# Performance work log

Measured on AMD Instinct MI355X. Metric: run time of the kernel, lower is better.

Reference implementation:

```python
import jax, jax.numpy as jnp
import numpy as np

POOL = 7
STRIDE = 16.0


def setup_inputs() -> dict:
    key = jax.random.key(0)
    k1, k2, k3, k4, k5 = jax.random.split(key, 5)
    image = jax.random.normal(k1, (1, 128, 128, 512), dtype=jnp.float32)
    N = 1000
    # RoIs in input-image pixel coords: (x_center, y_center, w, h)
    w = jax.random.uniform(k2, (N,), minval=32.0, maxval=480.0)
    h = jax.random.uniform(k3, (N,), minval=32.0, maxval=480.0)
    x0 = jax.random.uniform(k4, (N,), minval=0.0, maxval=1500.0)
    y0 = jax.random.uniform(k5, (N,), minval=0.0, maxval=1500.0)
    RoI = jnp.stack([x0 + w / 2, y0 + h / 2, w, h], axis=1).astype(jnp.float32)
    return {"image": image, "RoI_inImage": RoI}


def _axis_coords(start, size, pool, limit):
    """Half-pixel bilinear sample coords for resizing a [size]-long crop
    starting at `start` to `pool` samples (matches tf.image.resize bilinear).
    Returns (i0, i1, frac) each [N, pool]."""
    grid = (jnp.arange(pool, dtype=jnp.float32) + 0.5) / pool  # [pool]
    s = grid[None, :] * size[:, None] - 0.5                    # crop-relative
    s = jnp.clip(s, 0.0, size[:, None] - 1.0)
    f0 = jnp.floor(s)
    frac = s - f0
    f1 = jnp.minimum(f0 + 1.0, size[:, None] - 1.0)
    i0 = jnp.clip(start[:, None] + f0, 0, limit - 1).astype(jnp.int32)
    i1 = jnp.clip(start[:, None] + f1, 0, limit - 1).astype(jnp.int32)
    return i0, i1, frac


def _roi_pool(image, RoI):
    H, W = image.shape[1], image.shape[2]
    feat = image[0]  # [H, W, C]
    x, y, w, h = RoI[:, 0], RoI[:, 1], RoI[:, 2], RoI[:, 3]
    # integer crop bounds on the stride-16 feature map (non-differentiable)
    r = jax.lax.stop_gradient(jnp.round((x - w / 2) / STRIDE))   # col start
    c = jax.lax.stop_gradient(jnp.round((y - h / 2) / STRIDE))   # row start
    wq = jax.lax.stop_gradient(jnp.maximum(jnp.round(w / STRIDE), 1.0))
    hq = jax.lax.stop_gradient(jnp.maximum(jnp.round(h / STRIDE), 1.0))
    iy0, iy1, ly = _axis_coords(c, hq, POOL, H)  # rows   [N, P]
    ix0, ix1, lx = _axis_coords(r, wq, POOL, W)  # cols   [N, P]
    # gather 4 corners: [N, P, P, C]
    g = lambda iy, ix: feat[iy[:, :, None], ix[:, None, :]]
    ly_ = ly[:, :, None, None]
    lx_ = lx[:, None, :, None]
    out = ((1 - ly_) * (1 - lx_) * g(iy0, ix0)
           + (1 - ly_) * lx_ * g(iy0, ix1)
           + ly_ * (1 - lx_) * g(iy1, ix0)
           + ly_ * lx_ * g(iy1, ix1))
    N = RoI.shape[0]
    return out.reshape(1, N, POOL, POOL, feat.shape[-1])


def reference(image, RoI_inImage):
    return _roi_pool(image, RoI_inImage)
```

## Files before the change

### kernel.cpp

```cpp
#include <hip/hip_runtime.h>

#define POOL    7
#define RSTRIDE 16.0f
#define IMG_H   128
#define IMG_W   128
#define IMG_C   512
#define C4      (IMG_C / 4)

typedef float f4v __attribute__((ext_vector_type(4)));

template <bool SWIZZLE>
__global__ __launch_bounds__(128)
void roi_pool_kernel(const float* __restrict__ image,
                     const float* __restrict__ roi,
                     float* __restrict__ out, int N)
{
    int n, py;
    if (SWIZZLE) {
        const int per   = N >> 3;
        const int xcd   = blockIdx.x & 7;
        const int local = blockIdx.x >> 3;
        const int q     = local / POOL;
        n  = xcd * per + q;
        py = local - q * POOL;
    } else {
        n  = blockIdx.x / POOL;
        py = blockIdx.x - n * POOL;
    }

    const float x = roi[n * 4 + 0];
    const float y = roi[n * 4 + 1];
    const float w = roi[n * 4 + 2];
    const float h = roi[n * 4 + 3];

    const float r  = rintf((x - 0.5f * w) / RSTRIDE);
    const float c  = rintf((y - 0.5f * h) / RSTRIDE);
    const float wq = fmaxf(rintf(w / RSTRIDE), 1.0f);
    const float hq = fmaxf(rintf(h / RSTRIDE), 1.0f);

    float sy = (((float)py + 0.5f) / (float)POOL) * hq - 0.5f;
    sy = fminf(fmaxf(sy, 0.0f), hq - 1.0f);
    const float fy0 = floorf(sy);
    const float ly  = sy - fy0;
    const float fy1 = fminf(fy0 + 1.0f, hq - 1.0f);
    const int iy0 = (int)fminf(fmaxf(c + fy0, 0.0f), (float)(IMG_H - 1));
    const int iy1 = (int)fminf(fmaxf(c + fy1, 0.0f), (float)(IMG_H - 1));

    int   ix0[POOL], ix1[POOL];
    float w00[POOL], w01[POOL], w10[POOL], w11[POOL];
#pragma unroll
    for (int px = 0; px < POOL; ++px) {
        float sx = (((float)px + 0.5f) / (float)POOL) * wq - 0.5f;
        sx = fminf(fmaxf(sx, 0.0f), wq - 1.0f);
        const float fx0 = floorf(sx);
        const float lx  = sx - fx0;
        const float fx1 = fminf(fx0 + 1.0f, wq - 1.0f);
        ix0[px] = (int)fminf(fmaxf(r + fx0, 0.0f), (float)(IMG_W - 1)) * C4;
        ix1[px] = (int)fminf(fmaxf(r + fx1, 0.0f), (float)(IMG_W - 1)) * C4;
        w00[px] = (1.0f - ly) * (1.0f - lx);
        w01[px] = (1.0f - ly) * lx;
        w10[px] = ly * (1.0f - lx);
        w11[px] = ly * lx;
    }

    const int t = threadIdx.x;
    const f4v* row0 = (const f4v*)(image + (size_t)iy0 * IMG_W * IMG_C) + t;
    const f4v* row1 = (const f4v*)(image + (size_t)iy1 * IMG_W * IMG_C) + t;
    f4v* po = (f4v*)(out + ((size_t)n * (POOL * POOL) + (size_t)py * POOL) * IMG_C) + t;

    {
        f4v A[4], B[4], C[4], D[4];
#pragma unroll
        for (int i = 0; i < 4; ++i) {
            A[i] = row0[ix0[i]];
            B[i] = row0[ix1[i]];
            C[i] = row1[ix0[i]];
            D[i] = row1[ix1[i]];
        }
#pragma unroll
        for (int i = 0; i < 4; ++i) {
            po[i * C4] = w00[i] * A[i] + w01[i] * B[i] + w10[i] * C[i] + w11[i] * D[i];
        }
    }
    {
        f4v A[3], B[3], C[3], D[3];
#pragma unroll
        for (int i = 0; i < 3; ++i) {
            A[i] = row0[ix0[4 + i]];
            B[i] = row0[ix1[4 + i]];
            C[i] = row1[ix0[4 + i]];
            D[i] = row1[ix1[4 + i]];
        }
#pragma unroll
        for (int i = 0; i < 3; ++i) {
            po[(4 + i) * C4] = w00[4 + i] * A[i] + w01[4 + i] * B[i] +
                               w10[4 + i] * C[i] + w11[4 + i] * D[i];
        }
    }
}

extern "C" void kernel_launch(void* const* d_in, const int* in_sizes, int n_in,
                              void* d_out, int out_size, void* d_ws, size_t ws_size,
                              hipStream_t stream)
{
    const float* image = (const float*)d_in[0];
    const float* roi   = (const float*)d_in[1];
    float*       out   = (float*)d_out;

    const int N = in_sizes[1] / 4;
    const int blocks = N * POOL;

    if ((N & 7) == 0) {
        roi_pool_kernel<true><<<blocks, 128, 0, stream>>>(image, roi, out, N);
    } else {
        roi_pool_kernel<false><<<blocks, 128, 0, stream>>>(image, roi, out, N);
    }
}
```

Measured before the change: 150.2 us.

## Bin-sort RoIs by spatial location so each XCD handles nearby RoIs

Adds a single-block pre-pass that puts RoIs into 64 spatial bins by center, using a Morton-like bin index, with a shared-memory histogram and scan. The pooling kernel then reads RoIs through this order, so each XCD's contiguous chunk covers spatially nearby RoIs and shares image rows in its L2. The cost is an extra tiny kernel launch that serialises before the main kernel, plus an indirect load per block.

Result: no change. 152.1 us (+1.2%).

```diff
diff --git a/kernel.cpp b/kernel.cpp
--- a/kernel.cpp
+++ b/kernel.cpp
@@ -6,23 +6,61 @@
 #define IMG_W   128
 #define IMG_C   512
 #define C4      (IMG_C / 4)
+#define NBINS   64
 
 typedef float f4v __attribute__((ext_vector_type(4)));
 
-template <bool SWIZZLE>
+__device__ __forceinline__ int roi_bin(const float* __restrict__ roi, int i) {
+    const float x = roi[i * 4 + 0];
+    const float y = roi[i * 4 + 1];
+    const int cx = (int)fminf(fmaxf(x * (1.0f / RSTRIDE), 0.0f), 127.0f);
+    const int cy = (int)fminf(fmaxf(y * (1.0f / RSTRIDE), 0.0f), 127.0f);
+    const int bx = cx >> 4, by = cy >> 4;
+    return (by & 1) | ((bx & 1) << 1) | ((by & 2) << 1) |
+           ((bx & 2) << 2) | ((by & 4) << 2) | ((bx & 4) << 3);
+}
+
+__global__ __launch_bounds__(1024)
+void roi_sort_kernel(const float* __restrict__ roi, int N, int* __restrict__ order)
+{
+    __shared__ int cnt[NBINS];
+    const int t = threadIdx.x;
+    if (t < NBINS) cnt[t] = 0;
+    __syncthreads();
+    int mybin = -1;
+    if (t < N) { mybin = roi_bin(roi, t); atomicAdd(&cnt[mybin], 1); }
+    __syncthreads();
+    if (t < 64) {
+        int v = cnt[t];
+        int s = v;
+        #pragma unroll
+        for (int d = 1; d < 64; d <<= 1) {
+            int up = __shfl_up(s, d, 64);
+            if ((t & 63) >= d) s += up;
+        }
+        cnt[t] = s - v;
+    }
+    __syncthreads();
+    if (t < N) {
+        const int p = atomicAdd(&cnt[mybin], 1);
+        order[p] = t;
+    }
+}
+
+template <bool SORT>
 __global__ __launch_bounds__(128)
 void roi_pool_kernel(const float* __restrict__ image,
                      const float* __restrict__ roi,
-                     float* __restrict__ out, int N)
+                     float* __restrict__ out, int N,
+                     const int* __restrict__ order)
 {
     int n, py;
-    if (SWIZZLE) {
-        const int per   = N >> 3;
-        const int xcd   = blockIdx.x & 7;
-        const int local = blockIdx.x >> 3;
-        const int q     = local / POOL;
-        n  = xcd * per + q;
-        py = local - q * POOL;
+    if (SORT) {
+        const int xcd = blockIdx.x & 7;
+        const int j   = blockIdx.x >> 3;
+        const int q   = j / POOL;
+        py = j - q * POOL;
+        n  = order[xcd * (N >> 3) + q];
     } else {
         n  = blockIdx.x / POOL;
         py = blockIdx.x - n * POOL;
@@ -78,9 +116,8 @@
             D[i] = row1[ix1[i]];
         }
 #pragma unroll
-        for (int i = 0; i < 4; ++i) {
+        for (int i = 0; i < 4; ++i)
             po[i * C4] = w00[i] * A[i] + w01[i] * B[i] + w10[i] * C[i] + w11[i] * D[i];
-        }
     }
     {
         f4v A[3], B[3], C[3], D[3];
@@ -92,10 +129,9 @@
             D[i] = row1[ix1[4 + i]];
         }
 #pragma unroll
-        for (int i = 0; i < 3; ++i) {
+        for (int i = 0; i < 3; ++i)
             po[(4 + i) * C4] = w00[4 + i] * A[i] + w01[4 + i] * B[i] +
                                w10[4 + i] * C[i] + w11[4 + i] * D[i];
-        }
     }
 }
 
@@ -109,10 +145,14 @@
 
     const int N = in_sizes[1] / 4;
     const int blocks = N * POOL;
+    int* order = (int*)d_ws;
 
-    if ((N & 7) == 0) {
-        roi_pool_kernel<true><<<blocks, 128, 0, stream>>>(image, roi, out, N);
+    const bool sortable = ((N & 7) == 0) && N <= 1024 &&
+                          ws_size >= (size_t)N * sizeof(int);
+    if (sortable) {
+        roi_sort_kernel<<<1, 1024, 0, stream>>>(roi, N, order);
+        roi_pool_kernel<true><<<blocks, 128, 0, stream>>>(image, roi, out, N, order);
     } else {
-        roi_pool_kernel<false><<<blocks, 128, 0, stream>>>(image, roi, out, N);
+        roi_pool_kernel<false><<<blocks, 128, 0, stream>>>(image, roi, out, N, order);
     }
 }
```
